# Kernel optimization log

Measured on AMD Instinct MI355X. Metric: run time of the kernel, lower is better.

## Reference

```python
import jax, jax.numpy as jnp
import numpy as np

COMMITMENT_COST = 0.25


def setup_inputs() -> dict:
    key = jax.random.key(0)
    k1, k2 = jax.random.split(key)
    N, K, D = 65536, 8192, 64
    z_e = jax.random.normal(k1, (N, D), dtype=jnp.float32)
    # xavier_uniform for Embedding(K, D): limit = sqrt(6/(K+D))
    limit = float(np.sqrt(6.0 / (K + D)))
    codebook = jax.random.uniform(k2, (K, D), dtype=jnp.float32, minval=-limit, maxval=limit)
    return {"z_e": z_e, "codebook": codebook}


def reference(z_e, codebook):
    # Squared Euclidean distances; argmin over d^2 == argmin over cdist(p=2)
    x2 = jnp.sum(z_e * z_e, axis=-1, keepdims=True)            # [N,1]
    e2 = jnp.sum(codebook * codebook, axis=-1)                 # [K]
    d2 = x2 - 2.0 * (z_e @ codebook.T) + e2                    # [N,K]
    encoding_indices = jnp.argmin(d2, axis=-1)                 # [N] int

    z_q = codebook[encoding_indices]                           # [N,D] gather

    sg = jax.lax.stop_gradient
    codebook_loss = jnp.mean((z_q - sg(z_e)) ** 2)
    commitment_loss = jnp.mean((z_e - sg(z_q)) ** 2)
    vq_loss = codebook_loss + COMMITMENT_COST * commitment_loss

    # straight-through estimator
    z_q_st = z_e + sg(z_q - z_e)
    return z_q_st, vq_loss, encoding_indices
```

## Files before the change

kernel.cpp:

```cpp
#include <hip/hip_runtime.h>
#include <hip/hip_bf16.h>

#define N_PTS 65536
#define K_CB  8192
#define D_DIM 64
#define CAPS  63

typedef float f32x4 __attribute__((ext_vector_type(4)));
typedef short s16x8 __attribute__((ext_vector_type(8)));

typedef __attribute__((address_space(1))) const unsigned int gu32;
typedef __attribute__((address_space(3))) unsigned int lu32;

__device__ __forceinline__ unsigned bfpack2(float a, float b) {
    union { __hip_bfloat162 h2; unsigned u; } cv;
    cv.h2 = __float22bfloat162_rn(make_float2(a, b));
    return cv.u;
}

__device__ __forceinline__ void gl2lds16(const void* g, void* lds) {
    __builtin_amdgcn_global_load_lds((gu32*)g, (lu32*)lds, 16, 0, 0);
}

template <int CTRL>
__device__ __forceinline__ float dpp_fmax(float v) {
    int s = __builtin_amdgcn_update_dpp(0, __float_as_int(v), CTRL, 0xf, 0xf, true);
    return fmaxf(v, __int_as_float(s));
}

__global__ __launch_bounds__(256) void vq_pack(
        const float* __restrict__ cb, unsigned short* __restrict__ cbswz) {
    int g = blockIdx.x * 256 + threadIdx.x;
    int row = g >> 3, s = g & 7;
    int u = (s ^ (row & 7)) * 8;
    const float4* p = (const float4*)(cb + (size_t)row * D_DIM + u);
    float4 a = p[0], b = p[1];
    uint4 pk;
    pk.x = bfpack2(a.x, a.y); pk.y = bfpack2(a.z, a.w);
    pk.z = bfpack2(b.x, b.y); pk.w = bfpack2(b.z, b.w);
    *(uint4*)(cbswz + (size_t)row * 64 + s * 8) = pk;
}

__global__ __launch_bounds__(256) void vq_prep(
        const float* __restrict__ z, const float* __restrict__ cb,
        float* __restrict__ e2, float* __restrict__ x2, float* __restrict__ bmax) {
#pragma clang fp contract(off)
    __shared__ float sm[4];
    int b = blockIdx.x;
    int lane = threadIdx.x & 63;
    int wv = threadIdx.x >> 6;
    const float* src; float* dst; int row0;
    if (b < 128) { src = cb; dst = e2; row0 = b * 64 + wv * 16; }
    else         { src = z;  dst = x2; row0 = (b - 128) * 64 + wv * 16; }
    float lmax = 0.f;
    for (int r = 0; r < 16; ++r) {
        int row = row0 + r;
        float v = src[(size_t)row * D_DIM + lane];
        float w = v * v;
        float ra = w;
#pragma unroll
        for (int i = 1; i < 8; ++i) ra = ra + __shfl(w, lane + 8 * i, 64);
        float r0 = __shfl(ra, 0, 64), r1 = __shfl(ra, 1, 64),
              r2 = __shfl(ra, 2, 64), r3 = __shfl(ra, 3, 64),
              r4 = __shfl(ra, 4, 64), r5 = __shfl(ra, 5, 64),
              r6 = __shfl(ra, 6, 64), r7 = __shfl(ra, 7, 64);
        if (lane == 0) {
            float s = ((r0 + r1) + (r2 + r3)) + ((r4 + r5) + (r6 + r7));
            dst[row] = s;
            lmax = fmaxf(lmax, s);
        }
    }
    if (b < 128) {
        if (lane == 0) sm[wv] = lmax;
        __syncthreads();
        if (threadIdx.x == 0)
            bmax[b] = fmaxf(fmaxf(sm[0], sm[1]), fmaxf(sm[2], sm[3]));
    }
}

__device__ __forceinline__ void stage_chunk(
        const unsigned short* __restrict__ cbswz, const float* __restrict__ e2,
        unsigned short* bufb, float* e2hb, int kc, int w, int l) {
    const char* gbase = (const char*)(cbswz + (size_t)kc * 256 * 64);
#pragma unroll
    for (int j = 0; j < 4; ++j) {
        int off = j * 8192 + w * 1024;
        gl2lds16(gbase + off + l * 16, (char*)bufb + off);
    }
    if (w == 0)
        gl2lds16(e2 + kc * 256 + l * 4, e2hb);
}

__global__ __launch_bounds__(512, 4) void vq_coarse(
        const float* __restrict__ z, const unsigned short* __restrict__ cbswz,
        const float* __restrict__ e2, const float* __restrict__ x2,
        const float* __restrict__ bmax, int* __restrict__ cand) {
    __shared__ __align__(16) unsigned short pool[4][128 * 64];
    __shared__ __align__(16) float e2h[2][256];
    __shared__ int cntS[128];
    const int tid = threadIdx.x;
    const int w = tid >> 6, l = tid & 63, tx = l & 15, q = l >> 4;
    const int n0 = blockIdx.x * 128;

    if (tid < 128) cntS[tid] = 0;

#pragma unroll
    for (int i = 0; i < 2; ++i) {
        int lin = tid + 512 * i;
        int row = lin >> 3, u = lin & 7;
        const float4* p = (const float4*)(z + (size_t)(n0 + row) * D_DIM + u * 8);
        float4 a = p[0], b2 = p[1];
        uint4 pk;
        pk.x = bfpack2(a.x, a.y);   pk.y = bfpack2(a.z, a.w);
        pk.z = bfpack2(b2.x, b2.y); pk.w = bfpack2(b2.z, b2.w);
        *(uint4*)&pool[0][row * 64 + ((u ^ (row & 7)) * 8)] = pk;
    }

    float e2m;
    {
        float v = fmaxf(bmax[l], bmax[l + 64]);
#pragma unroll
        for (int m = 1; m < 64; m <<= 1) v = fmaxf(v, __shfl_xor(v, m, 64));
        e2m = v;
    }

    float halfW[4], A[4], M[4];
#pragma unroll
    for (int i = 0; i < 4; ++i) {
        int row = n0 + w * 16 + q * 4 + i;
        halfW[i] = 0.0175f * sqrtf(x2[row] * e2m) + 1e-4f;
        A[i] = 3.0e38f;
        M[i] = -3.4e38f;
    }
    float Amin = 3.0e38f;

    __syncthreads();
    s16x8 afr[2];
#pragma unroll
    for (int ks = 0; ks < 2; ++ks) {
        int row = w * 16 + tx;
        afr[ks] = *(const s16x8*)&pool[0][row * 64 + (((ks * 4 + q) ^ (tx & 7)) * 8)];
    }
    __syncthreads();

    stage_chunk(cbswz, e2, &pool[0][0], e2h[0], 0, w, l);
    __syncthreads();

    for (int it = 0; it < 33; ++it) {
        const int kc = (it < 32) ? it : 0;
        const int cur = it & 1;
        if (it < 32)
            stage_chunk(cbswz, e2, &pool[((it + 1) & 1) * 2][0], e2h[(it + 1) & 1],
                        (it + 1 < 32) ? it + 1 : 0, w, l);

        const unsigned short* cbb = &pool[cur * 2][0];
        const float* e2c = e2h[cur];
#pragma unroll 4
        for (int ct = 0; ct < 16; ++ct) {
            int crow = ct * 16 + tx;
            float bias = -0.5f * e2c[crow];
            s16x8 b0 = *(const s16x8*)&cbb[crow * 64 + ((q ^ (tx & 7)) * 8)];
            s16x8 b1 = *(const s16x8*)&cbb[crow * 64 + (((4 + q) ^ (tx & 7)) * 8)];
            f32x4 acc = {bias, bias, bias, bias};
            acc = __builtin_amdgcn_mfma_f32_16x16x32_bf16(afr[0], b0, acc, 0, 0, 0);
            acc = __builtin_amdgcn_mfma_f32_16x16x32_bf16(afr[1], b1, acc, 0, 0, 0);
            M[0] = fmaxf(M[0], acc[0]);
            M[1] = fmaxf(M[1], acc[1]);
            M[2] = fmaxf(M[2], acc[2]);
            M[3] = fmaxf(M[3], acc[3]);
            float amax = fmaxf(fmaxf(acc[0], acc[1]), fmaxf(acc[2], acc[3]));
            if (amax >= Amin) {
                int kglob = kc * 256 + crow;
#pragma unroll
                for (int r = 0; r < 4; ++r) {
                    if (acc[r] >= A[r]) {
                        int row = w * 16 + q * 4 + r;
                        int slot = atomicAdd(&cntS[row], 1);
                        if (slot < CAPS)
                            cand[(size_t)(n0 + row) * 64 + slot] = kglob;
                    }
                }
            }
        }
        if (it < 32) {
#pragma unroll
            for (int i = 0; i < 4; ++i) {
                float v = M[i];
                v = dpp_fmax<0xB1>(v);
                v = dpp_fmax<0x4E>(v);
                v = dpp_fmax<0x124>(v);
                v = dpp_fmax<0x128>(v);
                M[i] = v;
                A[i] = v - halfW[i];
            }
            Amin = fminf(fminf(A[0], A[1]), fminf(A[2], A[3]));
        }
        __syncthreads();
    }
    if (tid < 128) cand[(size_t)(n0 + tid) * 64 + 63] = cntS[tid];
}

__device__ __forceinline__ float exact_score(const float* zr, const float* __restrict__ cb,
                                             const float* __restrict__ e2, float x2v, int k) {
    const float4* c4 = (const float4*)(cb + (size_t)k * D_DIM);
    float g = 0.f;
#pragma unroll
    for (int j = 0; j < 16; ++j) {
        float4 v = c4[j];
        g = fmaf(zr[4 * j + 0], v.x, g);
        g = fmaf(zr[4 * j + 1], v.y, g);
        g = fmaf(zr[4 * j + 2], v.z, g);
        g = fmaf(zr[4 * j + 3], v.w, g);
    }
    return fmaf(-2.f, g, x2v) + e2[k];
}

__global__ __launch_bounds__(256, 2) void vq_rescore(
        const float* __restrict__ z, const float* __restrict__ cb,
        const float* __restrict__ e2, const float* __restrict__ x2,
        int* __restrict__ slots, float* __restrict__ idx_out,
        float* __restrict__ partials) {
    int tid = threadIdx.x;
    int n = blockIdx.x * 256 + tid;
    float zr[64];
    const float4* z4 = (const float4*)(z + (size_t)n * D_DIM);
#pragma unroll
    for (int i = 0; i < 16; ++i) {
        float4 v = z4[i];
        zr[4 * i] = v.x; zr[4 * i + 1] = v.y; zr[4 * i + 2] = v.z; zr[4 * i + 3] = v.w;
    }
    float x2v = x2[n];
    int cnt = slots[(size_t)n * 64 + 63];
    float bs = 3.4e38f; int bk = 0x7fffffff;
    if (cnt <= CAPS) {
        int i = 0;
        for (; i + 1 < cnt; i += 2) {
            int ka = slots[(size_t)n * 64 + i];
            int kb = slots[(size_t)n * 64 + i + 1];
            float sa = exact_score(zr, cb, e2, x2v, ka);
            float sb = exact_score(zr, cb, e2, x2v, kb);
            if (sa < bs || (sa == bs && ka < bk)) { bs = sa; bk = ka; }
            if (sb < bs || (sb == bs && kb < bk)) { bs = sb; bk = kb; }
        }
        if (i < cnt) {
            int k = slots[(size_t)n * 64 + i];
            float s = exact_score(zr, cb, e2, x2v, k);
            if (s < bs || (s == bs && k < bk)) { bs = s; bk = k; }
        }
    }
    unsigned long long mask = __ballot(cnt > CAPS);
    while (mask) {
        int src = __ffsll((long long)mask) - 1;
        mask &= (mask - 1);
        int rown = __shfl(n, src, 64);
        float x2s = __shfl(x2v, src, 64);
        float zs[64];
        const float4* zz = (const float4*)(z + (size_t)rown * D_DIM);
#pragma unroll
        for (int i = 0; i < 16; ++i) {
            float4 v = zz[i];
            zs[4 * i] = v.x; zs[4 * i + 1] = v.y; zs[4 * i + 2] = v.z; zs[4 * i + 3] = v.w;
        }
        float fb = 3.4e38f; int fk = 0x7fffffff;
        for (int k = (tid & 63); k < K_CB; k += 64) {
            float s = exact_score(zs, cb, e2, x2s, k);
            if (s < fb || (s == fb && k < fk)) { fb = s; fk = k; }
        }
#pragma unroll
        for (int m = 1; m < 64; m <<= 1) {
            float ov = __shfl_xor(fb, m, 64);
            int   ok = __shfl_xor(fk, m, 64);
            if (ov < fb || (ov == fb && ok < fk)) { fb = ov; fk = ok; }
        }
        if ((tid & 63) == src) { bs = fb; bk = fk; }
    }
    idx_out[n] = (float)bk;
    __threadfence_block();

    float lsum = 0.f;
    const float4* c4 = (const float4*)(cb + (size_t)bk * D_DIM);
    float4* o4 = (float4*)((float*)slots + (size_t)n * 64);
#pragma unroll
    for (int j = 0; j < 16; ++j) {
        float4 c = c4[j];
        float4 o;
        float d0 = c.x - zr[4 * j];     o.x = zr[4 * j]     + d0;
        float d1 = c.y - zr[4 * j + 1]; o.y = zr[4 * j + 1] + d1;
        float d2 = c.z - zr[4 * j + 2]; o.z = zr[4 * j + 2] + d2;
        float d3 = c.w - zr[4 * j + 3]; o.w = zr[4 * j + 3] + d3;
        lsum += d0 * d0 + d1 * d1 + d2 * d2 + d3 * d3;
        o4[j] = o;
    }
    __shared__ float red[256];
    red[tid] = lsum;
    __syncthreads();
    for (int s = 128; s > 0; s >>= 1) {
        if (tid < s) red[tid] += red[tid + s];
        __syncthreads();
    }
    if (tid == 0) partials[blockIdx.x] = red[0];
}

__global__ void vq_final(const float* __restrict__ partials, float* __restrict__ loss_out) {
    __shared__ float red[256];
    int tid = threadIdx.x;
    red[tid] = partials[tid];
    __syncthreads();
    for (int s = 128; s > 0; s >>= 1) {
        if (tid < s) red[tid] += red[tid + s];
        __syncthreads();
    }
    if (tid == 0) *loss_out = 1.25f * red[0] / (float)(N_PTS * D_DIM);
}

extern "C" void kernel_launch(void* const* d_in, const int* in_sizes, int n_in,
                              void* d_out, int out_size, void* d_ws, size_t ws_size,
                              hipStream_t stream) {
    const float* z  = (const float*)d_in[0];
    const float* cb = (const float*)d_in[1];
    float* out      = (float*)d_out;
    float* zq_out   = out;
    float* loss_out = out + (size_t)N_PTS * D_DIM;
    float* idx_out  = loss_out + 1;

    float* wsf = (float*)d_ws;
    float* partials = wsf;
    float* e2 = wsf + 256;
    float* x2 = wsf + 256 + K_CB;
    unsigned short* cbswz = (unsigned short*)(wsf + 256 + K_CB + N_PTS);

    int* cand = (int*)zq_out;
    float* bmax = idx_out;

    vq_pack   <<<K_CB * 8 / 256, 256, 0, stream>>>(cb, cbswz);
    vq_prep   <<<128 + N_PTS / 64, 256, 0, stream>>>(z, cb, e2, x2, bmax);
    vq_coarse <<<N_PTS / 128, 512, 0, stream>>>(z, cbswz, e2, x2, bmax, cand);
    vq_rescore<<<N_PTS / 256, 256, 0, stream>>>(z, cb, e2, x2, cand, idx_out, partials);
    vq_final  <<<1, 256, 0, stream>>>(partials, loss_out);
}
```

Measured before the change: 275.9 us.

## Split codebook tiles across wave pairs in coarse pass and pair threads in rescore

The coarse kernel now handles 64 rows per block, with two waves sharing each 16-row group and each taking half of every 128-entry codebook chunk. The two halves merge their running maxima through shared memory once per chunk. LDS per block is halved so more blocks can be resident, but each block streams the full codebook for half as many rows, which doubles total codebook traffic and adds a barrier-synchronised merge step. The rescore kernel assigns two threads per point, splitting the candidate list between them and combining results with a shuffle.

```diff
diff --git a/kernel.cpp b/kernel.cpp
--- a/kernel.cpp
+++ b/kernel.cpp
@@ -81,33 +81,33 @@
 __device__ __forceinline__ void stage_chunk(
         const unsigned short* __restrict__ cbswz, const float* __restrict__ e2,
         unsigned short* bufb, float* e2hb, int kc, int w, int l) {
-    const char* gbase = (const char*)(cbswz + (size_t)kc * 256 * 64);
-#pragma unroll
-    for (int j = 0; j < 4; ++j) {
+    const char* gbase = (const char*)(cbswz + (size_t)kc * 128 * 64);
+#pragma unroll
+    for (int j = 0; j < 2; ++j) {
         int off = j * 8192 + w * 1024;
         gl2lds16(gbase + off + l * 16, (char*)bufb + off);
     }
-    if (w == 0)
-        gl2lds16(e2 + kc * 256 + l * 4, e2hb);
-}
-
-__global__ __launch_bounds__(512, 4) void vq_coarse(
+    if (w == 0 && l < 32)
+        gl2lds16(e2 + (size_t)kc * 128 + l * 4, e2hb);
+}
+
+__global__ __launch_bounds__(512, 8) void vq_coarse(
         const float* __restrict__ z, const unsigned short* __restrict__ cbswz,
         const float* __restrict__ e2, const float* __restrict__ x2,
         const float* __restrict__ bmax, int* __restrict__ cand) {
-    __shared__ __align__(16) unsigned short pool[4][128 * 64];
-    __shared__ __align__(16) float e2h[2][256];
-    __shared__ int cntS[128];
+    __shared__ __align__(16) unsigned short pool[2][128 * 64];
+    __shared__ __align__(16) float e2h[2][128];
+    __shared__ __align__(16) float mrg[2][2][4][4][4];
+    __shared__ int cntS[64];
     const int tid = threadIdx.x;
     const int w = tid >> 6, l = tid & 63, tx = l & 15, q = l >> 4;
-    const int n0 = blockIdx.x * 128;
-
-    if (tid < 128) cntS[tid] = 0;
-
-#pragma unroll
-    for (int i = 0; i < 2; ++i) {
-        int lin = tid + 512 * i;
-        int row = lin >> 3, u = lin & 7;
+    const int rg = w >> 1, half = w & 1;
+    const int n0 = blockIdx.x * 64;
+
+    if (tid < 64) cntS[tid] = 0;
+
+    {
+        int row = tid >> 3, u = tid & 7;
         const float4* p = (const float4*)(z + (size_t)(n0 + row) * D_DIM + u * 8);
         float4 a = p[0], b2 = p[1];
         uint4 pk;
@@ -127,7 +127,7 @@
     float halfW[4], A[4], M[4];
 #pragma unroll
     for (int i = 0; i < 4; ++i) {
-        int row = n0 + w * 16 + q * 4 + i;
+        int row = n0 + rg * 16 + q * 4 + i;
         halfW[i] = 0.0175f * sqrtf(x2[row] * e2m) + 1e-4f;
         A[i] = 3.0e38f;
         M[i] = -3.4e38f;
@@ -138,25 +138,26 @@
     s16x8 afr[2];
 #pragma unroll
     for (int ks = 0; ks < 2; ++ks) {
-        int row = w * 16 + tx;
+        int row = rg * 16 + tx;
         afr[ks] = *(const s16x8*)&pool[0][row * 64 + (((ks * 4 + q) ^ (tx & 7)) * 8)];
     }
     __syncthreads();
 
-    stage_chunk(cbswz, e2, &pool[0][0], e2h[0], 0, w, l);
-    __syncthreads();
-
-    for (int it = 0; it < 33; ++it) {
-        const int kc = (it < 32) ? it : 0;
+    stage_chunk(cbswz, e2, pool[0], e2h[0], 0, w, l);
+    __syncthreads();
+
+    for (int it = 0; it < 65; ++it) {
+        const int kc = (it < 64) ? it : 0;
         const int cur = it & 1;
-        if (it < 32)
-            stage_chunk(cbswz, e2, &pool[((it + 1) & 1) * 2][0], e2h[(it + 1) & 1],
-                        (it + 1 < 32) ? it + 1 : 0, w, l);
-
-        const unsigned short* cbb = &pool[cur * 2][0];
+        if (it < 64)
+            stage_chunk(cbswz, e2, pool[cur ^ 1], e2h[cur ^ 1],
+                        (it + 1 < 64) ? it + 1 : 0, w, l);
+
+        const unsigned short* cbb = pool[cur];
         const float* e2c = e2h[cur];
-#pragma unroll 4
-        for (int ct = 0; ct < 16; ++ct) {
+#pragma unroll
+        for (int c4 = 0; c4 < 4; ++c4) {
+            int ct = half * 4 + c4;
             int crow = ct * 16 + tx;
             float bias = -0.5f * e2c[crow];
             s16x8 b0 = *(const s16x8*)&cbb[crow * 64 + ((q ^ (tx & 7)) * 8)];
@@ -168,13 +169,13 @@
             M[1] = fmaxf(M[1], acc[1]);
             M[2] = fmaxf(M[2], acc[2]);
             M[3] = fmaxf(M[3], acc[3]);
-            float amax = fmaxf(fmaxf(acc[0], acc[1]), fmaxf(acc[2], acc[3]));
+            float amax = fmaxf(fmaxf(fmaxf(acc[0], acc[1]), acc[2]), acc[3]);
             if (amax >= Amin) {
-                int kglob = kc * 256 + crow;
+                int kglob = kc * 128 + crow;
 #pragma unroll
                 for (int r = 0; r < 4; ++r) {
                     if (acc[r] >= A[r]) {
-                        int row = w * 16 + q * 4 + r;
+                        int row = rg * 16 + q * 4 + r;
                         int slot = atomicAdd(&cntS[row], 1);
                         if (slot < CAPS)
                             cand[(size_t)(n0 + row) * 64 + slot] = kglob;
@@ -182,7 +183,7 @@
                 }
             }
         }
-        if (it < 32) {
+        if (it < 64) {
 #pragma unroll
             for (int i = 0; i < 4; ++i) {
                 float v = M[i];
@@ -191,13 +192,23 @@
                 v = dpp_fmax<0x124>(v);
                 v = dpp_fmax<0x128>(v);
                 M[i] = v;
-                A[i] = v - halfW[i];
             }
+            if (tx == 0)
+                *(float4*)&mrg[it & 1][half][rg][q][0] = make_float4(M[0], M[1], M[2], M[3]);
+        }
+        __syncthreads();
+        if (it < 64) {
+            float4 om = *(const float4*)&mrg[it & 1][half ^ 1][rg][q][0];
+            M[0] = fmaxf(M[0], om.x);
+            M[1] = fmaxf(M[1], om.y);
+            M[2] = fmaxf(M[2], om.z);
+            M[3] = fmaxf(M[3], om.w);
+#pragma unroll
+            for (int i = 0; i < 4; ++i) A[i] = M[i] - halfW[i];
             Amin = fminf(fminf(A[0], A[1]), fminf(A[2], A[3]));
         }
-        __syncthreads();
-    }
-    if (tid < 128) cand[(size_t)(n0 + tid) * 64 + 63] = cntS[tid];
+    }
+    if (tid < 64) cand[(size_t)(n0 + tid) * 64 + 63] = cntS[tid];
 }
 
 __device__ __forceinline__ float exact_score(const float* zr, const float* __restrict__ cb,
@@ -215,13 +226,14 @@
     return fmaf(-2.f, g, x2v) + e2[k];
 }
 
-__global__ __launch_bounds__(256, 2) void vq_rescore(
+__global__ __launch_bounds__(512, 2) void vq_rescore(
         const float* __restrict__ z, const float* __restrict__ cb,
         const float* __restrict__ e2, const float* __restrict__ x2,
         int* __restrict__ slots, float* __restrict__ idx_out,
         float* __restrict__ partials) {
     int tid = threadIdx.x;
-    int n = blockIdx.x * 256 + tid;
+    int r = tid >> 1, half = tid & 1;
+    int n = blockIdx.x * 256 + r;
     float zr[64];
     const float4* z4 = (const float4*)(z + (size_t)n * D_DIM);
 #pragma unroll
@@ -233,22 +245,13 @@
     int cnt = slots[(size_t)n * 64 + 63];
     float bs = 3.4e38f; int bk = 0x7fffffff;
     if (cnt <= CAPS) {
-        int i = 0;
-        for (; i + 1 < cnt; i += 2) {
-            int ka = slots[(size_t)n * 64 + i];
-            int kb = slots[(size_t)n * 64 + i + 1];
-            float sa = exact_score(zr, cb, e2, x2v, ka);
-            float sb = exact_score(zr, cb, e2, x2v, kb);
-            if (sa < bs || (sa == bs && ka < bk)) { bs = sa; bk = ka; }
-            if (sb < bs || (sb == bs && kb < bk)) { bs = sb; bk = kb; }
-        }
-        if (i < cnt) {
+        for (int i = half; i < cnt; i += 2) {
             int k = slots[(size_t)n * 64 + i];
             float s = exact_score(zr, cb, e2, x2v, k);
             if (s < bs || (s == bs && k < bk)) { bs = s; bk = k; }
         }
     }
-    unsigned long long mask = __ballot(cnt > CAPS);
+    unsigned long long mask = __ballot(cnt > CAPS && half == 0);
     while (mask) {
         int src = __ffsll((long long)mask) - 1;
         mask &= (mask - 1);
@@ -274,25 +277,32 @@
         }
         if ((tid & 63) == src) { bs = fb; bk = fk; }
     }
-    idx_out[n] = (float)bk;
+    {
+        float ov = __shfl_xor(bs, 1, 64);
+        int   ok = __shfl_xor(bk, 1, 64);
+        if (ov < bs || (ov == bs && ok < bk)) { bs = ov; bk = ok; }
+    }
     __threadfence_block();
 
-    float lsum = 0.f;
-    const float4* c4 = (const float4*)(cb + (size_t)bk * D_DIM);
-    float4* o4 = (float4*)((float*)slots + (size_t)n * 64);
-#pragma unroll
-    for (int j = 0; j < 16; ++j) {
-        float4 c = c4[j];
-        float4 o;
-        float d0 = c.x - zr[4 * j];     o.x = zr[4 * j]     + d0;
-        float d1 = c.y - zr[4 * j + 1]; o.y = zr[4 * j + 1] + d1;
-        float d2 = c.z - zr[4 * j + 2]; o.z = zr[4 * j + 2] + d2;
-        float d3 = c.w - zr[4 * j + 3]; o.w = zr[4 * j + 3] + d3;
-        lsum += d0 * d0 + d1 * d1 + d2 * d2 + d3 * d3;
-        o4[j] = o;
-    }
     __shared__ float red[256];
-    red[tid] = lsum;
+    if (half == 0) {
+        idx_out[n] = (float)bk;
+        float lsum = 0.f;
+        const float4* c4 = (const float4*)(cb + (size_t)bk * D_DIM);
+        float4* o4 = (float4*)((float*)slots + (size_t)n * 64);
+#pragma unroll
+        for (int j = 0; j < 16; ++j) {
+            float4 c = c4[j];
+            float4 o;
+            float d0 = c.x - zr[4 * j];     o.x = zr[4 * j]     + d0;
+            float d1 = c.y - zr[4 * j + 1]; o.y = zr[4 * j + 1] + d1;
+            float d2 = c.z - zr[4 * j + 2]; o.z = zr[4 * j + 2] + d2;
+            float d3 = c.w - zr[4 * j + 3]; o.w = zr[4 * j + 3] + d3;
+            lsum += d0 * d0 + d1 * d1 + d2 * d2 + d3 * d3;
+            o4[j] = o;
+        }
+        red[r] = lsum;
+    }
     __syncthreads();
     for (int s = 128; s > 0; s >>= 1) {
         if (tid < s) red[tid] += red[tid + s];
@@ -334,7 +344,7 @@
 
     vq_pack   <<<K_CB * 8 / 256, 256, 0, stream>>>(cb, cbswz);
     vq_prep   <<<128 + N_PTS / 64, 256, 0, stream>>>(z, cb, e2, x2, bmax);
-    vq_coarse <<<N_PTS / 128, 512, 0, stream>>>(z, cbswz, e2, x2, bmax, cand);
-    vq_rescore<<<N_PTS / 256, 256, 0, stream>>>(z, cb, e2, x2, cand, idx_out, partials);
+    vq_coarse <<<N_PTS / 64, 512, 0, stream>>>(z, cbswz, e2, x2, bmax, cand);
+    vq_rescore<<<N_PTS / 256, 512, 0, stream>>>(z, cb, e2, x2, cand, idx_out, partials);
     vq_final  <<<1, 256, 0, stream>>>(partials, loss_out);
 }
```

New measurement: 305.5 us. 10.7% more time.

## Split VQ rescoring across four threads per row and trim coarse-pass overhead

Applied to the files above, without the earlier changes.

The rescore kernel now runs 1024-thread blocks with four lanes per query row. Each lane scores a strided subset of that row's candidates, and the lanes merge their results with an xor-shuffle argmin. The coarse kernel reads a precomputed -0.5*e2 array written by the prep kernel, fully unrolls its tile loop, and updates the pruning threshold only on the first and odd iterations, which cuts reduction work at the cost of a looser threshold and possibly more candidates. The aggressive launch bound on rescore may constrain registers and cause spills of the 64-float row buffer.

```diff
diff --git a/kernel.cpp b/kernel.cpp
--- a/kernel.cpp
+++ b/kernel.cpp
@@ -43,15 +43,16 @@
 
 __global__ __launch_bounds__(256) void vq_prep(
         const float* __restrict__ z, const float* __restrict__ cb,
-        float* __restrict__ e2, float* __restrict__ x2, float* __restrict__ bmax) {
+        float* __restrict__ e2, float* __restrict__ e2n,
+        float* __restrict__ x2, float* __restrict__ bmax) {
 #pragma clang fp contract(off)
     __shared__ float sm[4];
     int b = blockIdx.x;
     int lane = threadIdx.x & 63;
     int wv = threadIdx.x >> 6;
-    const float* src; float* dst; int row0;
-    if (b < 128) { src = cb; dst = e2; row0 = b * 64 + wv * 16; }
-    else         { src = z;  dst = x2; row0 = (b - 128) * 64 + wv * 16; }
+    const float* src; float* dst; int row0; bool iscb;
+    if (b < 128) { src = cb; dst = e2; row0 = b * 64 + wv * 16; iscb = true; }
+    else         { src = z;  dst = x2; row0 = (b - 128) * 64 + wv * 16; iscb = false; }
     float lmax = 0.f;
     for (int r = 0; r < 16; ++r) {
         int row = row0 + r;
@@ -67,6 +68,7 @@
         if (lane == 0) {
             float s = ((r0 + r1) + (r2 + r3)) + ((r4 + r5) + (r6 + r7));
             dst[row] = s;
+            if (iscb) e2n[row] = -0.5f * s;
             lmax = fmaxf(lmax, s);
         }
     }
@@ -79,7 +81,7 @@
 }
 
 __device__ __forceinline__ void stage_chunk(
-        const unsigned short* __restrict__ cbswz, const float* __restrict__ e2,
+        const unsigned short* __restrict__ cbswz, const float* __restrict__ e2n,
         unsigned short* bufb, float* e2hb, int kc, int w, int l) {
     const char* gbase = (const char*)(cbswz + (size_t)kc * 256 * 64);
 #pragma unroll
@@ -88,12 +90,12 @@
         gl2lds16(gbase + off + l * 16, (char*)bufb + off);
     }
     if (w == 0)
-        gl2lds16(e2 + kc * 256 + l * 4, e2hb);
+        gl2lds16(e2n + kc * 256 + l * 4, e2hb);
 }
 
 __global__ __launch_bounds__(512, 4) void vq_coarse(
         const float* __restrict__ z, const unsigned short* __restrict__ cbswz,
-        const float* __restrict__ e2, const float* __restrict__ x2,
+        const float* __restrict__ e2n, const float* __restrict__ x2,
         const float* __restrict__ bmax, int* __restrict__ cand) {
     __shared__ __align__(16) unsigned short pool[4][128 * 64];
     __shared__ __align__(16) float e2h[2][256];
@@ -143,22 +145,22 @@
     }
     __syncthreads();
 
-    stage_chunk(cbswz, e2, &pool[0][0], e2h[0], 0, w, l);
+    stage_chunk(cbswz, e2n, &pool[0][0], e2h[0], 0, w, l);
     __syncthreads();
 
     for (int it = 0; it < 33; ++it) {
         const int kc = (it < 32) ? it : 0;
         const int cur = it & 1;
         if (it < 32)
-            stage_chunk(cbswz, e2, &pool[((it + 1) & 1) * 2][0], e2h[(it + 1) & 1],
+            stage_chunk(cbswz, e2n, &pool[((it + 1) & 1) * 2][0], e2h[(it + 1) & 1],
                         (it + 1 < 32) ? it + 1 : 0, w, l);
 
         const unsigned short* cbb = &pool[cur * 2][0];
         const float* e2c = e2h[cur];
-#pragma unroll 4
+#pragma unroll
         for (int ct = 0; ct < 16; ++ct) {
             int crow = ct * 16 + tx;
-            float bias = -0.5f * e2c[crow];
+            float bias = e2c[crow];
             s16x8 b0 = *(const s16x8*)&cbb[crow * 64 + ((q ^ (tx & 7)) * 8)];
             s16x8 b1 = *(const s16x8*)&cbb[crow * 64 + (((4 + q) ^ (tx & 7)) * 8)];
             f32x4 acc = {bias, bias, bias, bias};
@@ -168,7 +170,7 @@
             M[1] = fmaxf(M[1], acc[1]);
             M[2] = fmaxf(M[2], acc[2]);
             M[3] = fmaxf(M[3], acc[3]);
-            float amax = fmaxf(fmaxf(acc[0], acc[1]), fmaxf(acc[2], acc[3]));
+            float amax = fmaxf(fmaxf(fmaxf(acc[0], acc[1]), acc[2]), acc[3]);
             if (amax >= Amin) {
                 int kglob = kc * 256 + crow;
 #pragma unroll
@@ -182,7 +184,7 @@
                 }
             }
         }
-        if (it < 32) {
+        if (it < 32 && ((it == 0) || (it & 1))) {
 #pragma unroll
             for (int i = 0; i < 4; ++i) {
                 float v = M[i];
@@ -215,13 +217,14 @@
     return fmaf(-2.f, g, x2v) + e2[k];
 }
 
-__global__ __launch_bounds__(256, 2) void vq_rescore(
+__global__ __launch_bounds__(1024, 4) void vq_rescore(
         const float* __restrict__ z, const float* __restrict__ cb,
         const float* __restrict__ e2, const float* __restrict__ x2,
         int* __restrict__ slots, float* __restrict__ idx_out,
         float* __restrict__ partials) {
     int tid = threadIdx.x;
-    int n = blockIdx.x * 256 + tid;
+    int r = tid >> 2, sub = tid & 3;
+    int n = blockIdx.x * 256 + r;
     float zr[64];
     const float4* z4 = (const float4*)(z + (size_t)n * D_DIM);
 #pragma unroll
@@ -233,22 +236,13 @@
     int cnt = slots[(size_t)n * 64 + 63];
     float bs = 3.4e38f; int bk = 0x7fffffff;
     if (cnt <= CAPS) {
-        int i = 0;
-        for (; i + 1 < cnt; i += 2) {
-            int ka = slots[(size_t)n * 64 + i];
-            int kb = slots[(size_t)n * 64 + i + 1];
-            float sa = exact_score(zr, cb, e2, x2v, ka);
-            float sb = exact_score(zr, cb, e2, x2v, kb);
-            if (sa < bs || (sa == bs && ka < bk)) { bs = sa; bk = ka; }
-            if (sb < bs || (sb == bs && kb < bk)) { bs = sb; bk = kb; }
-        }
-        if (i < cnt) {
+        for (int i = sub; i < cnt; i += 4) {
             int k = slots[(size_t)n * 64 + i];
             float s = exact_score(zr, cb, e2, x2v, k);
             if (s < bs || (s == bs && k < bk)) { bs = s; bk = k; }
         }
     }
-    unsigned long long mask = __ballot(cnt > CAPS);
+    unsigned long long mask = __ballot(cnt > CAPS && sub == 0);
     while (mask) {
         int src = __ffsll((long long)mask) - 1;
         mask &= (mask - 1);
@@ -274,25 +268,33 @@
         }
         if ((tid & 63) == src) { bs = fb; bk = fk; }
     }
-    idx_out[n] = (float)bk;
+#pragma unroll
+    for (int m = 1; m < 4; m <<= 1) {
+        float ov = __shfl_xor(bs, m, 64);
+        int   ok = __shfl_xor(bk, m, 64);
+        if (ov < bs || (ov == bs && ok < bk)) { bs = ov; bk = ok; }
+    }
     __threadfence_block();
 
-    float lsum = 0.f;
-    const float4* c4 = (const float4*)(cb + (size_t)bk * D_DIM);
-    float4* o4 = (float4*)((float*)slots + (size_t)n * 64);
-#pragma unroll
-    for (int j = 0; j < 16; ++j) {
-        float4 c = c4[j];
-        float4 o;
-        float d0 = c.x - zr[4 * j];     o.x = zr[4 * j]     + d0;
-        float d1 = c.y - zr[4 * j + 1]; o.y = zr[4 * j + 1] + d1;
-        float d2 = c.z - zr[4 * j + 2]; o.z = zr[4 * j + 2] + d2;
-        float d3 = c.w - zr[4 * j + 3]; o.w = zr[4 * j + 3] + d3;
-        lsum += d0 * d0 + d1 * d1 + d2 * d2 + d3 * d3;
-        o4[j] = o;
-    }
     __shared__ float red[256];
-    red[tid] = lsum;
+    if (sub == 0) {
+        idx_out[n] = (float)bk;
+        float lsum = 0.f;
+        const float4* c4 = (const float4*)(cb + (size_t)bk * D_DIM);
+        float4* o4 = (float4*)((float*)slots + (size_t)n * 64);
+#pragma unroll
+        for (int j = 0; j < 16; ++j) {
+            float4 c = c4[j];
+            float4 o;
+            float d0 = c.x - zr[4 * j];     o.x = zr[4 * j]     + d0;
+            float d1 = c.y - zr[4 * j + 1]; o.y = zr[4 * j + 1] + d1;
+            float d2 = c.z - zr[4 * j + 2]; o.z = zr[4 * j + 2] + d2;
+            float d3 = c.w - zr[4 * j + 3]; o.w = zr[4 * j + 3] + d3;
+            lsum += d0 * d0 + d1 * d1 + d2 * d2 + d3 * d3;
+            o4[j] = o;
+        }
+        red[r] = lsum;
+    }
     __syncthreads();
     for (int s = 128; s > 0; s >>= 1) {
         if (tid < s) red[tid] += red[tid + s];
@@ -325,16 +327,17 @@
 
     float* wsf = (float*)d_ws;
     float* partials = wsf;
-    float* e2 = wsf + 256;
-    float* x2 = wsf + 256 + K_CB;
-    unsigned short* cbswz = (unsigned short*)(wsf + 256 + K_CB + N_PTS);
+    float* e2  = wsf + 256;
+    float* e2n = wsf + 256 + K_CB;
+    float* x2  = wsf + 256 + 2 * K_CB;
+    unsigned short* cbswz = (unsigned short*)(wsf + 256 + 2 * K_CB + N_PTS);
 
     int* cand = (int*)zq_out;
     float* bmax = idx_out;
 
     vq_pack   <<<K_CB * 8 / 256, 256, 0, stream>>>(cb, cbswz);
-    vq_prep   <<<128 + N_PTS / 64, 256, 0, stream>>>(z, cb, e2, x2, bmax);
-    vq_coarse <<<N_PTS / 128, 512, 0, stream>>>(z, cbswz, e2, x2, bmax, cand);
-    vq_rescore<<<N_PTS / 256, 256, 0, stream>>>(z, cb, e2, x2, cand, idx_out, partials);
+    vq_prep   <<<128 + N_PTS / 64, 256, 0, stream>>>(z, cb, e2, e2n, x2, bmax);
+    vq_coarse <<<N_PTS / 128, 512, 0, stream>>>(z, cbswz, e2n, x2, bmax, cand);
+    vq_rescore<<<N_PTS / 256, 1024, 0, stream>>>(z, cb, e2, x2, cand, idx_out, partials);
     vq_final  <<<1, 256, 0, stream>>>(partials, loss_out);
 }
```

Result: slower. 326.8 us (+18.5%).
